# Kernel tuning notes

Measured on AMD Instinct MI355X. Metric: run time of the kernel, lower is better.

Reference implementation:

```python
import jax, jax.numpy as jnp
import numpy as np

NUM_CLUSTERS = 64
NUM_ITERS = 3
TEMPERATURE = 0.1
CENTER_EMA = 0.99


def _l2norm(x, eps=1e-12):
    n = jnp.linalg.norm(x, axis=-1, keepdims=True)
    return x / jnp.maximum(n, eps)


def setup_inputs() -> dict:
    key = jax.random.key(0)
    k1, k2 = jax.random.split(key)
    B, N, d = 16, 4096, 768
    features = jax.random.normal(k1, (B, N, d), dtype=jnp.float32)
    centers = jax.random.normal(k2, (NUM_CLUSTERS, d), dtype=jnp.float32)
    return {"features": features, "centers": centers}


def reference(features, centers):
    B, N, d = features.shape
    K = centers.shape[0]
    M = B * N  # single-device: M_total == M_local

    features_norm = _l2norm(features)          # [B, N, d]
    centers_n = _l2norm(centers)               # [K, d]

    logits = jnp.einsum('bnd,kd->bnk', features_norm, centers_n) / TEMPERATURE
    Q = jnp.exp(logits.astype(jnp.float32).reshape(M, K).T)  # [K, M]

    Q = Q / jnp.maximum(Q.sum(), 1e-12)
    for _ in range(NUM_ITERS):
        row_sums = Q.sum(axis=1, keepdims=True)              # [K, 1]
        Q = Q / (jnp.maximum(row_sums, 1e-12) * float(K))
        col_sums = Q.sum(axis=0, keepdims=True)              # [1, M]
        Q = Q / (jnp.maximum(col_sums, 1e-12) * float(M))

    assignments = (Q * float(M)).T.reshape(B, N, K).astype(features.dtype)

    # EMA center update
    Q_flat = assignments.reshape(M, K)
    feat_flat = features_norm.reshape(M, d)
    weighted = jnp.einsum('mk,md->kd', Q_flat, feat_flat)    # [K, d]
    mass = Q_flat.sum(axis=0)                                # [K]
    new_centers = _l2norm(weighted / jnp.maximum(mass, 1e-6)[:, None])
    updated = CENTER_EMA * centers_n + (1.0 - CENTER_EMA) * new_centers
    updated = _l2norm(updated)

    return assignments, updated
```

## Files before the change

kernel.cpp:

```cpp
#include <hip/hip_runtime.h>
#include <hip/hip_bf16.h>

#define M_TOTAL 65536
#define DIM 768
#define KC 64
#define INV_T 10.0f

#define DT 128
#define MB 64
#define CH 8
#define MSEG 128

#define LOGITS_BLOCKS (M_TOTAL / 64)
#define SROWS 128
#define SINK_BLOCKS (M_TOTAL / SROWS)
#define PSG_ROWS 64

typedef __attribute__((ext_vector_type(4))) float f32x4;
typedef __attribute__((ext_vector_type(8))) short bf16x8;
typedef __attribute__((ext_vector_type(4))) unsigned short u16x4;

__device__ __forceinline__ short f2bf(float f) {
    __hip_bfloat16 h = __float2bfloat16(f);
    union { __hip_bfloat16 h; short s; } u; u.h = h;
    return u.s;
}

__global__ __launch_bounds__(256) void k_centers(const float* __restrict__ centers,
                                                 float* __restrict__ cn,
                                                 short* __restrict__ cnbf,
                                                 float* __restrict__ psg) {
    int k = blockIdx.x, tid = threadIdx.x;
    psg[k * 256 + tid] = 0.f;
    float ss = 0.f;
    for (int i = tid; i < DIM; i += 256) { float v = centers[k * DIM + i]; ss += v * v; }
    __shared__ float red[4];
    for (int o = 32; o; o >>= 1) ss += __shfl_xor(ss, o);
    if ((tid & 63) == 0) red[tid >> 6] = ss;
    __syncthreads();
    ss = red[0] + red[1] + red[2] + red[3];
    float inv = 1.0f / fmaxf(sqrtf(ss), 1e-12f);
    for (int i = tid; i < DIM; i += 256) {
        float v = centers[k * DIM + i] * inv;
        cn[k * DIM + i] = v;
        cnbf[k * DIM + i] = f2bf(v);
    }
}

__global__ __launch_bounds__(256) void k_logits(const float* __restrict__ F,
                                                const short* __restrict__ cnbf,
                                                float* __restrict__ E,
                                                float* __restrict__ invn,
                                                float* __restrict__ PSG0) {
    __shared__ float fbuf[3][4][1024];
    __shared__ float bsr[4][KC];
    int tid = threadIdx.x;
    int wave = tid >> 6, lane = tid & 63;
    int l15 = lane & 15, lhi = lane >> 4;
    int rowbase = blockIdx.x * 64;

    int srow_l = lane >> 4;
    int c4 = lane & 15;

#define STAGE(t_, b_)                                                                     \
    do {                                                                                  \
        _Pragma("unroll") for (int i_ = 0; i_ < 4; ++i_) {                                \
            int r_ = i_ * 4 + srow_l;                                \
            const float* src_ = F + (size_t)(rowbase + wave * 16 + r_) * DIM + (t_) * 64  \
                                + (((c4 ^ (r_ & 7)) << 2));                               \
            float* dst_ = &fbuf[b_][wave][i_ * 256];                                      \
            __builtin_amdgcn_global_load_lds(                                             \
                (const __attribute__((address_space(1))) void*)src_,                      \
                (__attribute__((address_space(3))) void*)dst_, 16, 0, 0);                 \
        }                                                                                 \
    } while (0)

    STAGE(0, 0);
    STAGE(1, 1);

    f32x4 acc[4];
#pragma unroll
    for (int n = 0; n < 4; ++n) acc[n] = (f32x4){0.f, 0.f, 0.f, 0.f};
    float ss = 0.f;

    const short* Bb = cnbf + (size_t)l15 * DIM + lhi * 8;
    int swz = (l15 & 7) << 2;

#pragma unroll
    for (int t = 0; t < 12; ++t) {
        bf16x8 b[8];
#pragma unroll
        for (int n = 0; n < 4; ++n) {
            b[n * 2]     = *(const bf16x8*)(Bb + (size_t)n * 16 * DIM + t * 64);
            b[n * 2 + 1] = *(const bf16x8*)(Bb + (size_t)n * 16 * DIM + t * 64 + 32);
        }
        if (t + 2 < 12) {
            STAGE(t + 2, (t + 2) % 3);
            asm volatile("s_waitcnt vmcnt(4)" ::: "memory");
        } else {
            asm volatile("s_waitcnt vmcnt(0)" ::: "memory");
        }
        __builtin_amdgcn_sched_barrier(0);
        const float* cb = &fbuf[t % 3][wave][l15 * 64];
#pragma unroll
        for (int kk = 0; kk < 2; ++kk) {
            int c0s = (kk * 32 + lhi * 8) ^ swz;
            f32x4 fa = *(const f32x4*)(cb + c0s);
            f32x4 fb2 = *(const f32x4*)(cb + (c0s ^ 4));
            ss += fa[0] * fa[0] + fa[1] * fa[1] + fa[2] * fa[2] + fa[3] * fa[3]
                + fb2[0] * fb2[0] + fb2[1] * fb2[1] + fb2[2] * fb2[2] + fb2[3] * fb2[3];
            bf16x8 af;
            af[0] = f2bf(fa[0]); af[1] = f2bf(fa[1]); af[2] = f2bf(fa[2]); af[3] = f2bf(fa[3]);
            af[4] = f2bf(fb2[0]); af[5] = f2bf(fb2[1]); af[6] = f2bf(fb2[2]); af[7] = f2bf(fb2[3]);
#pragma unroll
            for (int n = 0; n < 4; ++n)
                acc[n] = __builtin_amdgcn_mfma_f32_16x16x32_bf16(af, b[n * 2 + kk], acc[n], 0, 0, 0);
        }
    }
#undef STAGE

    ss += __shfl_xor(ss, 16);
    ss += __shfl_xor(ss, 32);
    float inv = 1.0f / fmaxf(sqrtf(ss), 1e-12f);
    int growbase = rowbase + wave * 16;
    if (lane < 16) invn[growbase + lane] = inv;

    float sc[4];
#pragma unroll
    for (int j = 0; j < 4; ++j) sc[j] = __shfl(inv, lhi * 4 + j) * INV_T;

    float colp[4] = {0.f, 0.f, 0.f, 0.f};
#pragma unroll
    for (int n = 0; n < 4; ++n) {
#pragma unroll
        for (int j = 0; j < 4; ++j) {
            float e = expf(acc[n][j] * sc[j]);
            int row = lhi * 4 + j;
            E[(size_t)(growbase + row) * KC + ((n * 16 + l15) ^ (row << 2))] = e;
            colp[n] += e;
        }
    }
#pragma unroll
    for (int n = 0; n < 4; ++n) {
        colp[n] += __shfl_xor(colp[n], 16);
        colp[n] += __shfl_xor(colp[n], 32);
    }
    if (lane < 16) {
#pragma unroll
        for (int n = 0; n < 4; ++n) bsr[wave][n * 16 + lane] = colp[n];
    }
    __syncthreads();
    if (tid < KC)
        atomicAdd(&PSG0[(size_t)(blockIdx.x >> 4) * KC + tid],
                  bsr[0][tid] + bsr[1][tid] + bsr[2][tid] + bsr[3][tid]);
}

template <int MODE>
__global__ __launch_bounds__(256) void k_sink(const float* __restrict__ E,
                                              const float* __restrict__ Rprev,
                                              const float* __restrict__ PSGprev,
                                              const float* __restrict__ invn,
                                              float* __restrict__ c,
                                              float* __restrict__ PSGnext,
                                              float* __restrict__ Rout,
                                              float* __restrict__ Aout,
                                              short* __restrict__ QbfT) {
    __shared__ float tile[SROWS * KC];
    __shared__ float sbuf[SROWS];
    __shared__ float Rlds[KC];
    __shared__ float bacc[4][KC];
    int tid = threadIdx.x, lane = tid & 63, wave = tid >> 6;
    int m0 = blockIdx.x * SROWS;

#pragma unroll
    for (int i = 0; i < 8; ++i) {
        const float* src = E + (size_t)(m0 + i * 16 + wave * 4 + (lane >> 4)) * KC + (lane & 15) * 4;
        float* dst = tile + (i * 16 + wave * 4) * KC;
        __builtin_amdgcn_global_load_lds((const __attribute__((address_space(1))) void*)src,
                                         (__attribute__((address_space(3))) void*)dst, 16, 0, 0);
    }

    {
        int k = tid & 63, g = tid >> 6;
        float s = 0.f;
#pragma unroll
        for (int p = 0; p < PSG_ROWS / 4; ++p) s += PSGprev[(size_t)(g + p * 4) * KC + k];
        bacc[g][k] = s;
        __syncthreads();
        if (tid < KC) {
            float sk = bacc[0][k] + bacc[1][k] + bacc[2][k] + bacc[3][k];
            float r;
            if (MODE == 0) {
                float tot = sk;
                for (int o = 32; o; o >>= 1) tot += __shfl_xor(tot, o);
                float S = fmaxf(tot, 1e-12f);
                r = (1.0f / S) / (fmaxf(sk / S, 1e-12f) * 64.0f);
            } else {
                float rp = Rprev[k];
                r = rp / (fmaxf(rp * sk, 1e-12f) * 64.0f);
            }
            Rlds[k] = r;
            if (MODE != 2) Rout[k] = r;
        }
    }
    __syncthreads();

    if (tid < SROWS) {
        const float* rp = tile + tid * KC;
        const f32x4* R4 = (const f32x4*)Rlds;
        int sw = tid & 15;
        f32x4 a = {0.f, 0.f, 0.f, 0.f};
#pragma unroll
        for (int j = 0; j < 16; ++j)
            a += *(const f32x4*)(rp + ((j ^ sw) << 2)) * R4[j];
        sbuf[tid] = a[0] + a[1] + a[2] + a[3];
    }
    __syncthreads();

    float Rl = Rlds[lane];
    float wacc = 0.f;
    int rbase = wave * 32;
    short qbuf[32];
#pragma unroll
    for (int r = 0; r < 32; ++r) {
        int rr = rbase + r;
        int m = m0 + rr;
        float e = tile[rr * KC + (lane ^ ((rr & 15) << 2))];
        float s = sbuf[rr];
        float cold = (MODE == 0) ? 1.0f : c[m];
        float cnew = cold / (fmaxf(cold * s, 1e-12f) * 65536.0f);
        if (MODE == 2) {
            float a = e * Rl * cnew * 65536.0f;
            Aout[(size_t)m * KC + lane] = a;
            qbuf[r] = f2bf(a * invn[m]);
            wacc += a;
        } else {
            if (lane == 0) c[m] = cnew;
            wacc += e * cnew;
        }
    }
    if (MODE == 2) {
        unsigned u[16];
#pragma unroll
        for (int i = 0; i < 16; ++i)
            u[i] = (unsigned)(unsigned short)qbuf[2 * i] | ((unsigned)(unsigned short)qbuf[2 * i + 1] << 16);
        uint4* dst = (uint4*)(QbfT + (size_t)lane * M_TOTAL + m0 + rbase);
#pragma unroll
        for (int i = 0; i < 4; ++i)
            dst[i] = make_uint4(u[4 * i], u[4 * i + 1], u[4 * i + 2], u[4 * i + 3]);
    }
    bacc[wave][lane] = wacc;
    __syncthreads();
    if (tid < KC)
        atomicAdd(&PSGnext[(size_t)(blockIdx.x >> 3) * KC + tid],
                  bacc[0][tid] + bacc[1][tid] + bacc[2][tid] + bacc[3][tid]);
}

__global__ __launch_bounds__(256) void k_weighted(const float* __restrict__ F,
                                                  const short* __restrict__ QbfT,
                                                  float* __restrict__ P) {
    __shared__ short ldsF[DT * MB];
    int tid = threadIdx.x;
    int dt = blockIdx.x;
    int ms = blockIdx.y;
    int wave = tid >> 6, lane = tid & 63;
    int l15 = lane & 15, lhi = lane >> 4;

    int m0 = ms * (MB * CH);
    int d0 = dt * DT;

    f32x4 acc[4][2];
#pragma unroll
    for (int kt = 0; kt < 4; ++kt)
#pragma unroll
        for (int ds = 0; ds < 2; ++ds) acc[kt][ds] = (f32x4){0.f, 0.f, 0.f, 0.f};

    int f_dq = (tid & 31) * 4;
    int f_m8 = (tid >> 5) * 8;

    float4 rf[8];
#define LOADCH(mb_)                                                                       \
    do {                                                                                  \
        _Pragma("unroll") for (int j = 0; j < 8; ++j)                                     \
            rf[j] = *(const float4*)(F + (size_t)((mb_) + f_m8 + j) * DIM + d0 + f_dq);   \
    } while (0)

    LOADCH(m0);
    for (int ch = 0; ch < CH; ++ch) {
        int mb = m0 + ch * MB;
        __syncthreads();
#pragma unroll
        for (int i = 0; i < 4; ++i) {
            int d = f_dq + i;
            uint4 w;
            w.x = (unsigned)(unsigned short)f2bf(rf[0][i]) | ((unsigned)(unsigned short)f2bf(rf[1][i]) << 16);
            w.y = (unsigned)(unsigned short)f2bf(rf[2][i]) | ((unsigned)(unsigned short)f2bf(rf[3][i]) << 16);
            w.z = (unsigned)(unsigned short)f2bf(rf[4][i]) | ((unsigned)(unsigned short)f2bf(rf[5][i]) << 16);
            w.w = (unsigned)(unsigned short)f2bf(rf[6][i]) | ((unsigned)(unsigned short)f2bf(rf[7][i]) << 16);
            int byte = (d * (MB * 2) + f_m8 * 2) ^ ((d & 7) << 4);
            *(uint4*)((char*)ldsF + byte) = w;
        }
        __syncthreads();
        if (ch + 1 < CH) LOADCH(mb + MB);
#pragma unroll
        for (int h = 0; h < 2; ++h) {
            bf16x8 afr[4];
#pragma unroll
            for (int kt = 0; kt < 4; ++kt)
                afr[kt] = *(const bf16x8*)(QbfT + (size_t)(kt * 16 + l15) * M_TOTAL
                                           + mb + h * 32 + lhi * 8);
#pragma unroll
            for (int ds = 0; ds < 2; ++ds) {
                int d = wave * 32 + ds * 16 + l15;
                int byte = (d * (MB * 2) + (h * 32 + lhi * 8) * 2) ^ ((d & 7) << 4);
                bf16x8 bfr = *(bf16x8*)((char*)ldsF + byte);
#pragma unroll
                for (int kt = 0; kt < 4; ++kt)
                    acc[kt][ds] = __builtin_amdgcn_mfma_f32_16x16x32_bf16(afr[kt], bfr, acc[kt][ds], 0, 0, 0);
            }
        }
    }
#undef LOADCH

    float* Pb = P + (size_t)ms * (KC * DIM) + d0;
#pragma unroll
    for (int kt = 0; kt < 4; ++kt)
#pragma unroll
        for (int ds = 0; ds < 2; ++ds) {
            int d = wave * 32 + ds * 16 + l15;
#pragma unroll
            for (int r4 = 0; r4 < 4; ++r4) {
                int k = kt * 16 + lhi * 4 + r4;
                Pb[(size_t)k * DIM + d] = acc[kt][ds][r4];
            }
        }
}

__global__ __launch_bounds__(256) void k_final(const float* __restrict__ P,
                                               const float* __restrict__ PSGM,
                                               const float* __restrict__ cn,
                                               float* __restrict__ outC) {
    int k = blockIdx.x, tid = threadIdx.x;
    __shared__ float red[4];

    float msum = (tid < PSG_ROWS) ? PSGM[(size_t)tid * KC + k] : 0.f;
    for (int o = 32; o; o >>= 1) msum += __shfl_xor(msum, o);
    if ((tid & 63) == 0) red[tid >> 6] = msum;
    __syncthreads();
    float mk = fmaxf(red[0] + red[1] + red[2] + red[3], 1e-6f);
    __syncthreads();

    float w[3];
#pragma unroll
    for (int g = 0; g < 3; ++g) {
        int d = tid + g * 256;
        const float* pp = P + (size_t)k * DIM + d;
        float s0 = 0.f, s1 = 0.f, s2 = 0.f, s3 = 0.f;
        size_t stride = (size_t)KC * DIM;
#pragma unroll 4
        for (int msg = 0; msg < MSEG; msg += 4) {
            s0 += pp[(size_t)msg * stride];
            s1 += pp[(size_t)(msg + 1) * stride];
            s2 += pp[(size_t)(msg + 2) * stride];
            s3 += pp[(size_t)(msg + 3) * stride];
        }
        w[g] = ((s0 + s1) + (s2 + s3)) / mk;
    }

    float ss = w[0] * w[0] + w[1] * w[1] + w[2] * w[2];
    for (int o = 32; o; o >>= 1) ss += __shfl_xor(ss, o);
    if ((tid & 63) == 0) red[tid >> 6] = ss;
    __syncthreads();
    ss = red[0] + red[1] + red[2] + red[3];
    float n1 = fmaxf(sqrtf(ss), 1e-12f);
    __syncthreads();

    float u0 = 0.99f * cn[k * DIM + tid]       + 0.01f * (w[0] / n1);
    float u1 = 0.99f * cn[k * DIM + tid + 256] + 0.01f * (w[1] / n1);
    float u2 = 0.99f * cn[k * DIM + tid + 512] + 0.01f * (w[2] / n1);
    float ss2 = u0 * u0 + u1 * u1 + u2 * u2;
    for (int o = 32; o; o >>= 1) ss2 += __shfl_xor(ss2, o);
    if ((tid & 63) == 0) red[tid >> 6] = ss2;
    __syncthreads();
    ss2 = red[0] + red[1] + red[2] + red[3];
    float n2 = fmaxf(sqrtf(ss2), 1e-12f);

    outC[k * DIM + tid]       = u0 / n2;
    outC[k * DIM + tid + 256] = u1 / n2;
    outC[k * DIM + tid + 512] = u2 / n2;
}

extern "C" void kernel_launch(void* const* d_in, const int* in_sizes, int n_in,
                              void* d_out, int out_size, void* d_ws, size_t ws_size,
                              hipStream_t stream) {
    const float* F = (const float*)d_in[0];
    const float* centers = (const float*)d_in[1];
    float* out = (float*)d_out;
    float* A = out;
    float* outC = out + (size_t)M_TOTAL * KC;

    float* w = (float*)d_ws;
    float* cn   = w;
    short* cnbf = (short*)(w + 49152);
    float* R0   = w + 73728;
    float* R1   = w + 73792;
    float* invn = w + 74048;
    float* cbuf = w + 139584;
    float* E    = w + 205120;
    short* QbfT = (short*)(w + 4399424);
    float* PSG  = w + 6496576;
    float* PSG0 = PSG;
    float* PSG1 = PSG + 4096;
    float* PSG2 = PSG + 8192;
    float* PSGM = PSG + 12288;
    float* partial = w + 6520000;

    k_centers<<<KC, 256, 0, stream>>>(centers, cn, cnbf, PSG);
    k_logits<<<LOGITS_BLOCKS, 256, 0, stream>>>(F, cnbf, E, invn, PSG0);
    k_sink<0><<<SINK_BLOCKS, 256, 0, stream>>>(E, nullptr, PSG0, invn, cbuf, PSG1, R0, A, QbfT);
    k_sink<1><<<SINK_BLOCKS, 256, 0, stream>>>(E, R0, PSG1, invn, cbuf, PSG2, R1, A, QbfT);
    k_sink<2><<<SINK_BLOCKS, 256, 0, stream>>>(E, R1, PSG2, invn, cbuf, PSGM, nullptr, A, QbfT);

    dim3 wgrid(DIM / DT, MSEG);
    k_weighted<<<wgrid, 256, 0, stream>>>(F, QbfT, partial);
    k_final<<<KC, 256, 0, stream>>>(partial, PSGM, cn, outC);
}
```

Baseline: 162.2 us.

## Coalesce QbfT stores via LDS transpose and prefetch Q fragments in weighted GEMM

The sinkhorn output kernel now stages the bf16 Q values for each block in a padded shared tile and writes QbfT with row-contiguous 16-byte stores, instead of each lane writing scattered 64-byte strips. The weighted-sum kernel double-buffers the Q fragment loads in registers, issuing them for the next chunk alongside the feature loads so global latency overlaps the MFMA work. In exchange it adds an extra barrier, reuses the tile buffer as scratch, and raises register pressure from the two 8-fragment buffers.

```diff
diff --git a/kernel.cpp b/kernel.cpp
--- a/kernel.cpp
+++ b/kernel.cpp
@@ -239,18 +239,30 @@
             wacc += e * cnew;
         }
     }
+    bacc[wave][lane] = wacc;
+    __syncthreads();
+
     if (MODE == 2) {
-        unsigned u[16];
-#pragma unroll
-        for (int i = 0; i < 16; ++i)
-            u[i] = (unsigned)(unsigned short)qbuf[2 * i] | ((unsigned)(unsigned short)qbuf[2 * i + 1] << 16);
-        uint4* dst = (uint4*)(QbfT + (size_t)lane * M_TOTAL + m0 + rbase);
-#pragma unroll
-        for (int i = 0; i < 4; ++i)
-            dst[i] = make_uint4(u[4 * i], u[4 * i + 1], u[4 * i + 2], u[4 * i + 3]);
-    }
-    bacc[wave][lane] = wacc;
-    __syncthreads();
+        short* qT = (short*)tile;
+#pragma unroll
+        for (int i = 0; i < 4; ++i) {
+            unsigned a0 = (unsigned)(unsigned short)qbuf[8 * i]     | ((unsigned)(unsigned short)qbuf[8 * i + 1] << 16);
+            unsigned a1 = (unsigned)(unsigned short)qbuf[8 * i + 2] | ((unsigned)(unsigned short)qbuf[8 * i + 3] << 16);
+            unsigned a2 = (unsigned)(unsigned short)qbuf[8 * i + 4] | ((unsigned)(unsigned short)qbuf[8 * i + 5] << 16);
+            unsigned a3 = (unsigned)(unsigned short)qbuf[8 * i + 6] | ((unsigned)(unsigned short)qbuf[8 * i + 7] << 16);
+            *(uint4*)(qT + lane * 130 + rbase + i * 8) = make_uint4(a0, a1, a2, a3);
+        }
+        __syncthreads();
+        int k4 = tid >> 4;
+        int c16 = tid & 15;
+#pragma unroll
+        for (int pass = 0; pass < 4; ++pass) {
+            int k = pass * 16 + k4;
+            *(uint4*)(QbfT + (size_t)k * M_TOTAL + m0 + c16 * 8) =
+                *(const uint4*)(qT + k * 130 + c16 * 8);
+        }
+    }
+
     if (tid < KC)
         atomicAdd(&PSGnext[(size_t)(blockIdx.x >> 3) * KC + tid],
                   bacc[0][tid] + bacc[1][tid] + bacc[2][tid] + bacc[3][tid]);
@@ -279,47 +291,58 @@
     int f_m8 = (tid >> 5) * 8;
 
     float4 rf[8];
+    bf16x8 qA[8], qB[8];
+
 #define LOADCH(mb_)                                                                       \
     do {                                                                                  \
         _Pragma("unroll") for (int j = 0; j < 8; ++j)                                     \
             rf[j] = *(const float4*)(F + (size_t)((mb_) + f_m8 + j) * DIM + d0 + f_dq);   \
     } while (0)
 
+#define QLOAD(mb_, ARR)                                                                   \
+    do {                                                                                  \
+        _Pragma("unroll") for (int h_ = 0; h_ < 2; ++h_)                                  \
+            _Pragma("unroll") for (int kt_ = 0; kt_ < 4; ++kt_)                           \
+                ARR[h_ * 4 + kt_] = *(const bf16x8*)(QbfT                                 \
+                    + (size_t)(kt_ * 16 + l15) * M_TOTAL + (mb_) + h_ * 32 + lhi * 8);    \
+    } while (0)
+
+#define BODY(ch_, QC, QN)                                                                 \
+    {                                                                                     \
+        int mb_ = m0 + (ch_) * MB;                                                        \
+        __syncthreads();                                                                  \
+        _Pragma("unroll") for (int i = 0; i < 4; ++i) {                                   \
+            int d = f_dq + i;                                                             \
+            uint4 w;                                                                      \
+            w.x = (unsigned)(unsigned short)f2bf(rf[0][i]) | ((unsigned)(unsigned short)f2bf(rf[1][i]) << 16); \
+            w.y = (unsigned)(unsigned short)f2bf(rf[2][i]) | ((unsigned)(unsigned short)f2bf(rf[3][i]) << 16); \
+            w.z = (unsigned)(unsigned short)f2bf(rf[4][i]) | ((unsigned)(unsigned short)f2bf(rf[5][i]) << 16); \
+            w.w = (unsigned)(unsigned short)f2bf(rf[6][i]) | ((unsigned)(unsigned short)f2bf(rf[7][i]) << 16); \
+            int byte = (d * (MB * 2) + f_m8 * 2) ^ ((d & 7) << 4);                        \
+            *(uint4*)((char*)ldsF + byte) = w;                                            \
+        }                                                                                 \
+        __syncthreads();                                                                  \
+        if ((ch_) + 1 < CH) { LOADCH(mb_ + MB); QLOAD(mb_ + MB, QN); }                    \
+        _Pragma("unroll") for (int h = 0; h < 2; ++h) {                                   \
+            _Pragma("unroll") for (int ds = 0; ds < 2; ++ds) {                            \
+                int d = wave * 32 + ds * 16 + l15;                                        \
+                int byte = (d * (MB * 2) + (h * 32 + lhi * 8) * 2) ^ ((d & 7) << 4);      \
+                bf16x8 bfr = *(bf16x8*)((char*)ldsF + byte);                              \
+                _Pragma("unroll") for (int kt = 0; kt < 4; ++kt)                          \
+                    acc[kt][ds] = __builtin_amdgcn_mfma_f32_16x16x32_bf16(                \
+                        QC[h * 4 + kt], bfr, acc[kt][ds], 0, 0, 0);                       \
+            }                                                                             \
+        }                                                                                 \
+    }
+
     LOADCH(m0);
-    for (int ch = 0; ch < CH; ++ch) {
-        int mb = m0 + ch * MB;
-        __syncthreads();
-#pragma unroll
-        for (int i = 0; i < 4; ++i) {
-            int d = f_dq + i;
-            uint4 w;
-            w.x = (unsigned)(unsigned short)f2bf(rf[0][i]) | ((unsigned)(unsigned short)f2bf(rf[1][i]) << 16);
-            w.y = (unsigned)(unsigned short)f2bf(rf[2][i]) | ((unsigned)(unsigned short)f2bf(rf[3][i]) << 16);
-            w.z = (unsigned)(unsigned short)f2bf(rf[4][i]) | ((unsigned)(unsigned short)f2bf(rf[5][i]) << 16);
-            w.w = (unsigned)(unsigned short)f2bf(rf[6][i]) | ((unsigned)(unsigned short)f2bf(rf[7][i]) << 16);
-            int byte = (d * (MB * 2) + f_m8 * 2) ^ ((d & 7) << 4);
-            *(uint4*)((char*)ldsF + byte) = w;
-        }
-        __syncthreads();
-        if (ch + 1 < CH) LOADCH(mb + MB);
-#pragma unroll
-        for (int h = 0; h < 2; ++h) {
-            bf16x8 afr[4];
-#pragma unroll
-            for (int kt = 0; kt < 4; ++kt)
-                afr[kt] = *(const bf16x8*)(QbfT + (size_t)(kt * 16 + l15) * M_TOTAL
-                                           + mb + h * 32 + lhi * 8);
-#pragma unroll
-            for (int ds = 0; ds < 2; ++ds) {
-                int d = wave * 32 + ds * 16 + l15;
-                int byte = (d * (MB * 2) + (h * 32 + lhi * 8) * 2) ^ ((d & 7) << 4);
-                bf16x8 bfr = *(bf16x8*)((char*)ldsF + byte);
-#pragma unroll
-                for (int kt = 0; kt < 4; ++kt)
-                    acc[kt][ds] = __builtin_amdgcn_mfma_f32_16x16x32_bf16(afr[kt], bfr, acc[kt][ds], 0, 0, 0);
-            }
-        }
-    }
+    QLOAD(m0, qA);
+    for (int cc = 0; cc < CH; cc += 2) {
+        BODY(cc, qA, qB);
+        BODY(cc + 1, qB, qA);
+    }
+#undef BODY
+#undef QLOAD
 #undef LOADCH
 
     float* Pb = P + (size_t)ms * (KC * DIM) + d0;
```

Result: no change. 161.4 us (-0.5%).
